# Kernel tuning notes

Measured on AMD Instinct MI355X. Metric: run time of the kernel, lower is better.

The kernel has to match this reference:

```python
import jax, jax.numpy as jnp
import numpy as np

TT_IN = (8, 8, 8, 8)
TT_OUT = (8, 8, 8, 8)
TT_RANKS = (1, 32, 32, 32, 1)
BATCH = 4096
N_IN = int(np.prod(TT_IN))     # 4096
N_OUT = int(np.prod(TT_OUT))   # 4096
KERNEL_LEN = int(sum(TT_RANKS[k] * TT_IN[k] * TT_OUT[k] * TT_RANKS[k + 1]
                     for k in range(len(TT_IN))))  # 135168


def setup_inputs() -> dict:
    key = jax.random.key(0)
    kx, kk = jax.random.split(key)
    x = jax.random.normal(kx, (BATCH, N_IN), dtype=jnp.float32)
    # flat packed TT cores (the layer stores all cores in one 1-D weight)
    kernel = 0.02 * jax.random.normal(kk, (KERNEL_LEN,), dtype=jnp.float32)
    bias = jnp.zeros((N_OUT,), dtype=jnp.float32)
    return {"x": x, "kernel": kernel, "bias": bias}


def reference(x, kernel, bias):
    # Faithful translation of TensorTrainDense.call: iterate cores k = d-1 .. 0,
    # slicing the flat kernel from index 0 (matching the original code exactly).
    batch = x.shape[0]
    res = x
    idx = 0
    for k in range(len(TT_IN) - 1, -1, -1):
        m = TT_IN[k] * TT_RANKS[k + 1]   # contraction dim
        n = TT_RANKS[k] * TT_OUT[k]      # output dim of this core
        core = kernel[idx:idx + m * n].reshape(m, n)
        res = res.reshape(-1, m) @ core              # (-1, r_k*out_k)
        res = res.reshape(-1, TT_OUT[k]).T           # (out_k, -1)
        idx += m * n
    res = res.reshape(-1, batch).T                   # (batch, prod(out))
    return res + bias
```

## Files before the change

### kernel.cpp

```cpp
#include <hip/hip_runtime.h>
#include <hip/hip_bf16.h>

typedef unsigned short u16;
typedef __attribute__((ext_vector_type(8))) short  bf16x8;
typedef __attribute__((ext_vector_type(8))) u16    u16x8;
typedef __attribute__((ext_vector_type(4))) float  fx4;

#define OFF_C0 0
#define OFF_C1 2048
#define OFF_C2 67584
#define OFF_C3 133120

static __device__ __forceinline__ u16 f2bf(float f) {
  union { __hip_bfloat16 h; u16 u; } cv;
  cv.h = __float2bfloat16(f);
  return cv.u;
}
static __device__ __forceinline__ float bf2f(u16 u) {
  union { u16 u; __hip_bfloat16 h; } cv;
  cv.u = u;
  return __bfloat162float(cv.h);
}

__global__ void build_w34T(const float* __restrict__ ker, float* __restrict__ w34T) {
  int t = blockIdx.x * 256 + threadIdx.x;
  int i34 = t & 63, c = t >> 6;
  int a2 = c >> 6, o3 = (c >> 3) & 7, o4 = c & 7;
  int i3 = i34 >> 3, i4 = i34 & 7;
  float s = 0.f;
#pragma unroll 8
  for (int a3 = 0; a3 < 32; ++a3) {
    float k1 = ker[OFF_C1 + (i3 * 32 + a3) * 256 + a2 * 8 + o3];
    float k0 = ker[OFF_C0 + i4 * 256 + a3 * 8 + o4];
    s += k1 * k0;
  }
  w34T[c * 64 + i34] = s;
}

__global__ void build_w234t2(const float* __restrict__ ker, const float* __restrict__ w34T,
                             u16* __restrict__ w234t) {
  int t = blockIdx.x * 256 + threadIdx.x;
  int i234 = t & 511, g = t >> 9;
  int a1 = g >> 3, o3 = g & 7;
  int i2 = i234 >> 6, i34 = i234 & 63;
  float acc[8][8];
#pragma unroll
  for (int a = 0; a < 8; ++a)
#pragma unroll
    for (int b = 0; b < 8; ++b) acc[a][b] = 0.f;
  for (int a2 = 0; a2 < 32; ++a2) {
    float w[8];
#pragma unroll
    for (int o4 = 0; o4 < 8; ++o4)
      w[o4] = w34T[(a2 * 64 + o3 * 8 + o4) * 64 + i34];
#pragma unroll
    for (int o2 = 0; o2 < 8; ++o2) {
      float c2 = ker[OFF_C2 + (i2 * 32 + a2) * 256 + a1 * 8 + o2];
#pragma unroll
      for (int o4 = 0; o4 < 8; ++o4) acc[o2][o4] += c2 * w[o4];
    }
  }
#pragma unroll
  for (int o2 = 0; o2 < 8; ++o2) {
    int cg = a1 * 64 + o2 * 8 + o3;
#pragma unroll
    for (int o4 = 0; o4 < 8; ++o4)
      w234t[(cg * 8 + o4) * 512 + i234] = f2bf(acc[o2][o4]);
  }
}

__global__ void build_wt2(const float* __restrict__ ker, const u16* __restrict__ w234t,
                          u16* __restrict__ wt) {
  int t = blockIdx.x * 256 + threadIdx.x;
  int i234 = t & 511, j234 = t >> 9;
  float acc[8][8];
#pragma unroll
  for (int a = 0; a < 8; ++a)
#pragma unroll
    for (int b = 0; b < 8; ++b) acc[a][b] = 0.f;
  for (int a1 = 0; a1 < 32; ++a1) {
    float w = bf2f(w234t[(a1 * 512 + j234) * 512 + i234]);
#pragma unroll
    for (int i1 = 0; i1 < 8; ++i1) {
      const float* c3 = ker + OFF_C3 + (i1 * 32 + a1) * 8;
#pragma unroll
      for (int o1 = 0; o1 < 8; ++o1) acc[i1][o1] += c3[o1] * w;
    }
  }
#pragma unroll
  for (int o1 = 0; o1 < 8; ++o1)
#pragma unroll
    for (int i1 = 0; i1 < 8; ++i1)
      wt[(size_t)(o1 * 512 + j234) * 4096 + i1 * 512 + i234] = f2bf(acc[i1][o1]);
}

__device__ __forceinline__ void gld16(const void* g, void* l) {
  __builtin_amdgcn_global_load_lds((const __attribute__((address_space(1))) void*)g,
                                   (__attribute__((address_space(3))) void*)l, 16, 0, 0);
}

__global__ __launch_bounds__(512, 2) void gemm_f32a(const float* __restrict__ X, const u16* __restrict__ Bt,
                                                    const float* __restrict__ bias, float* __restrict__ C) {
  __shared__ __align__(16) float shA[24576];
  __shared__ __align__(16) u16   shB[24576];

  const int tid = threadIdx.x;
  const int lane = tid & 63;
  const int wave = tid >> 6;
  const int wm = wave >> 2, wn = wave & 3;
  const int fr = lane & 15, fg = lane >> 4;

  const int bid = blockIdx.x;
  const int wg = (bid & 7) * 32 + (bid >> 3);
  const int bm = (wg >> 4) * 256, bn = (wg & 15) * 256;

  size_t agA[4];
#pragma unroll
  for (int L = 0; L < 4; ++L) {
    const int r = L * 64 + (tid >> 3);
    agA[L] = (size_t)(bm + r) * 4096 + (((tid & 7) ^ (r & 7)) * 4);
  }
  size_t agB[2];
#pragma unroll
  for (int L = 0; L < 2; ++L) {
    const int r = L * 128 + (tid >> 2);
    agB[L] = (size_t)(bn + r) * 4096 + (((tid & 3) ^ ((r >> 1) & 3)) * 8);
  }
  const int ldsWA = wave * 256;
  const int ldsWB = wave * 512;

  int aoff[8][2], boff[4];
#pragma unroll
  for (int m = 0; m < 8; ++m) {
    const int R = wm * 128 + m * 16 + fr;
#pragma unroll
    for (int h = 0; h < 2; ++h)
      aoff[m][h] = R * 32 + (((fg * 2 + h) ^ (R & 7)) * 4);
  }
#pragma unroll
  for (int n = 0; n < 4; ++n) {
    const int R = wn * 64 + n * 16 + fr;
    boff[n] = R * 32 + ((fg ^ ((R >> 1) & 3)) * 8);
  }

  fx4 acc[8][4];
#pragma unroll
  for (int m = 0; m < 8; ++m)
#pragma unroll
    for (int n = 0; n < 4; ++n) acc[m][n] = (fx4){0.f, 0.f, 0.f, 0.f};

#define STAGE(buf, tt) do { const int k_ = ((tt) & 127) * 32; \
    float* a_ = shA + (buf) * 8192 + ldsWA; u16* b_ = shB + (buf) * 8192 + ldsWB; \
    gld16(X + agA[0] + k_, a_); \
    gld16(X + agA[1] + k_, a_ + 2048); \
    gld16(X + agA[2] + k_, a_ + 4096); \
    gld16(X + agA[3] + k_, a_ + 6144); \
    gld16(Bt + agB[0] + k_, b_); \
    gld16(Bt + agB[1] + k_, b_ + 4096); } while (0)

  STAGE(0, 0);
  STAGE(1, 1);
  asm volatile("s_waitcnt vmcnt(6)" ::: "memory");
  __builtin_amdgcn_s_barrier();

  int p = 0;
  for (int t = 0; t < 128; ++t) {
    const int ps = p + 2 >= 3 ? p - 1 : p + 2;
    const float* Ap = shA + p * 8192;
    const u16*   Bp = shB + p * 8192;

    bf16x8 bv[4];
#pragma unroll
    for (int n = 0; n < 4; ++n) bv[n] = *(const bf16x8*)(Bp + boff[n]);

    bf16x8 av[8];
#pragma unroll
    for (int m = 0; m < 8; ++m) {
      fx4 lo = *(const fx4*)(Ap + aoff[m][0]);
      fx4 hi = *(const fx4*)(Ap + aoff[m][1]);
      u16 tmp[8];
#pragma unroll
      for (int q = 0; q < 4; ++q) tmp[q] = f2bf(lo[q]);
#pragma unroll
      for (int q = 0; q < 4; ++q) tmp[4 + q] = f2bf(hi[q]);
      av[m] = *(const bf16x8*)tmp;
    }

    STAGE(ps, t + 2);

    __builtin_amdgcn_s_setprio(1);
#pragma unroll
    for (int m = 0; m < 8; ++m)
#pragma unroll
      for (int n = 0; n < 4; ++n)
        acc[m][n] = __builtin_amdgcn_mfma_f32_16x16x32_bf16(av[m], bv[n], acc[m][n], 0, 0, 0);
    __builtin_amdgcn_s_setprio(0);

    asm volatile("s_waitcnt vmcnt(6)" ::: "memory");
    __builtin_amdgcn_s_barrier();
    p = p + 1 >= 3 ? 0 : p + 1;
  }

  const int crow0 = bm + wm * 128 + fg * 4;
  const int ccol0 = bn + wn * 64 + fr;
#pragma unroll
  for (int n = 0; n < 4; ++n) {
    const int col = ccol0 + n * 16;
    const float bvl = bias[col];
#pragma unroll
    for (int mf = 0; mf < 8; ++mf) {
      const int r0 = crow0 + mf * 16;
#pragma unroll
      for (int q = 0; q < 4; ++q)
        C[(size_t)(r0 + q) * 4096 + col] = acc[mf][n][q] + bvl;
    }
  }
#undef STAGE
}

extern "C" void kernel_launch(void* const* d_in, const int* in_sizes, int n_in,
                              void* d_out, int out_size, void* d_ws, size_t ws_size,
                              hipStream_t stream) {
  const float* x    = (const float*)d_in[0];
  const float* ker  = (const float*)d_in[1];
  const float* bias = (const float*)d_in[2];
  float* out = (float*)d_out;

  char* ws = (char*)d_ws;
  u16*  wt    = (u16*)ws;
  u16*  w234t = (u16*)(ws + 33554432);
  float* w34T = (float*)(ws + 50331648);

  build_w34T  <<<512, 256, 0, stream>>>(ker, w34T);
  build_w234t2<<<512, 256, 0, stream>>>(ker, w34T, w234t);
  build_wt2   <<<1024, 256, 0, stream>>>(ker, w234t, wt);
  gemm_f32a   <<<256, 512, 0, stream>>>(x, wt, bias, out);
}
```

Before: 192.2 us.

## Convert X tile to bf16 once on load into LDS instead of per-wave

The fp32 A tile used to be copied straight into LDS with direct-to-LDS loads, and every wave then converted its fragments to bf16 after each LDS read. Now each thread loads its fp32 slice of X into registers, converts it to bf16 once and writes it to a half-size bf16 LDS buffer, so the MFMA loop reads bf16 directly. This is meant to remove redundant conversions and halve LDS traffic and footprint for A. In exchange the A loads go through VGPRs, which adds register pressure and an extra LDS write plus lgkmcnt wait before every barrier.

```diff
diff --git a/kernel.cpp b/kernel.cpp
--- a/kernel.cpp
+++ b/kernel.cpp
@@ -99,10 +99,10 @@
                                    (__attribute__((address_space(3))) void*)l, 16, 0, 0);
 }
 
-__global__ __launch_bounds__(512, 2) void gemm_f32a(const float* __restrict__ X, const u16* __restrict__ Bt,
+__global__ __launch_bounds__(512, 2) void gemm_xf32(const float* __restrict__ X, const u16* __restrict__ Bt,
                                                     const float* __restrict__ bias, float* __restrict__ C) {
-  __shared__ __align__(16) float shA[24576];
-  __shared__ __align__(16) u16   shB[24576];
+  __shared__ __align__(16) u16 shA[24576];
+  __shared__ __align__(16) u16 shB[24576];
 
   const int tid = threadIdx.x;
   const int lane = tid & 63;
@@ -114,28 +114,23 @@
   const int wg = (bid & 7) * 32 + (bid >> 3);
   const int bm = (wg >> 4) * 256, bn = (wg & 15) * 256;
 
-  size_t agA[4];
-#pragma unroll
-  for (int L = 0; L < 4; ++L) {
-    const int r = L * 64 + (tid >> 3);
-    agA[L] = (size_t)(bm + r) * 4096 + (((tid & 7) ^ (r & 7)) * 4);
-  }
-  size_t agB[2];
-#pragma unroll
-  for (int L = 0; L < 2; ++L) {
-    const int r = L * 128 + (tid >> 2);
-    agB[L] = (size_t)(bn + r) * 4096 + (((tid & 3) ^ ((r >> 1) & 3)) * 8);
-  }
-  const int ldsWA = wave * 256;
+  const int r0 = tid >> 2, r1 = r0 + 128, sl = tid & 3;
+  const size_t aglb0 = (size_t)(bm + r0) * 4096 + (sl ^ ((r0 >> 1) & 3)) * 8;
+  const size_t aglb1 = (size_t)(bm + r1) * 4096 + (sl ^ ((r1 >> 1) & 3)) * 8;
+  const int adst0 = r0 * 32 + sl * 8;
+  const int adst1 = r1 * 32 + sl * 8;
+
+  const int srow = tid >> 2;
+  const int sco = (((tid & 3) ^ ((tid >> 3) & 3)) * 8);
+  const size_t agB0 = (size_t)(bn + srow) * 4096 + sco;
+  const size_t agB1 = agB0 + (size_t)128 * 4096;
   const int ldsWB = wave * 512;
 
-  int aoff[8][2], boff[4];
+  int aoff[8], boff[4];
 #pragma unroll
   for (int m = 0; m < 8; ++m) {
     const int R = wm * 128 + m * 16 + fr;
-#pragma unroll
-    for (int h = 0; h < 2; ++h)
-      aoff[m][h] = R * 32 + (((fg * 2 + h) ^ (R & 7)) * 4);
+    aoff[m] = R * 32 + ((fg ^ ((R >> 1) & 3)) * 8);
   }
 #pragma unroll
   for (int n = 0; n < 4; ++n) {
@@ -149,44 +144,48 @@
 #pragma unroll
     for (int n = 0; n < 4; ++n) acc[m][n] = (fx4){0.f, 0.f, 0.f, 0.f};
 
-#define STAGE(buf, tt) do { const int k_ = ((tt) & 127) * 32; \
-    float* a_ = shA + (buf) * 8192 + ldsWA; u16* b_ = shB + (buf) * 8192 + ldsWB; \
-    gld16(X + agA[0] + k_, a_); \
-    gld16(X + agA[1] + k_, a_ + 2048); \
-    gld16(X + agA[2] + k_, a_ + 4096); \
-    gld16(X + agA[3] + k_, a_ + 6144); \
-    gld16(Bt + agB[0] + k_, b_); \
-    gld16(Bt + agB[1] + k_, b_ + 4096); } while (0)
-
-  STAGE(0, 0);
-  STAGE(1, 1);
-  asm volatile("s_waitcnt vmcnt(6)" ::: "memory");
+  fx4 axl0, axh0, axl1, axh1;
+
+#define ALOAD(tt) do { const int k_ = ((tt) & 127) * 32; \
+    axl0 = *(const fx4*)(X + aglb0 + k_);  axh0 = *(const fx4*)(X + aglb0 + k_ + 4); \
+    axl1 = *(const fx4*)(X + aglb1 + k_);  axh1 = *(const fx4*)(X + aglb1 + k_ + 4); } while (0)
+#define AWRITE(buf) do { \
+    u16 t0[8], t1[8]; \
+    _Pragma("unroll") for (int q = 0; q < 4; ++q) { t0[q] = f2bf(axl0[q]); t0[4 + q] = f2bf(axh0[q]); \
+                                                    t1[q] = f2bf(axl1[q]); t1[4 + q] = f2bf(axh1[q]); } \
+    u16* ab_ = shA + (buf) * 8192; \
+    *(u16x8*)(ab_ + adst0) = *(const u16x8*)t0; \
+    *(u16x8*)(ab_ + adst1) = *(const u16x8*)t1; } while (0)
+#define STAGE_B(buf, tt) do { const int k_ = ((tt) & 127) * 32; \
+    u16* b_ = shB + (buf) * 8192 + ldsWB; \
+    gld16(Bt + agB0 + k_, b_); \
+    gld16(Bt + agB1 + k_, b_ + 4096); } while (0)
+
+  ALOAD(0);
+  STAGE_B(0, 0);
+  asm volatile("s_waitcnt vmcnt(2)" ::: "memory");
+  AWRITE(0);
+  ALOAD(1);
+  STAGE_B(1, 1);
+  asm volatile("s_waitcnt vmcnt(2)" ::: "memory");
+  AWRITE(1);
+  asm volatile("s_waitcnt lgkmcnt(0)" ::: "memory");
   __builtin_amdgcn_s_barrier();
 
   int p = 0;
   for (int t = 0; t < 128; ++t) {
-    const int ps = p + 2 >= 3 ? p - 1 : p + 2;
-    const float* Ap = shA + p * 8192;
-    const u16*   Bp = shB + p * 8192;
-
-    bf16x8 bv[4];
+    const int p2 = p + 2 >= 3 ? p - 1 : p + 2;
+    const u16* Ap = shA + p * 8192;
+    const u16* Bp = shB + p * 8192;
+
+    bf16x8 av[8], bv[4];
+#pragma unroll
+    for (int m = 0; m < 8; ++m) av[m] = *(const bf16x8*)(Ap + aoff[m]);
 #pragma unroll
     for (int n = 0; n < 4; ++n) bv[n] = *(const bf16x8*)(Bp + boff[n]);
 
-    bf16x8 av[8];
-#pragma unroll
-    for (int m = 0; m < 8; ++m) {
-      fx4 lo = *(const fx4*)(Ap + aoff[m][0]);
-      fx4 hi = *(const fx4*)(Ap + aoff[m][1]);
-      u16 tmp[8];
-#pragma unroll
-      for (int q = 0; q < 4; ++q) tmp[q] = f2bf(lo[q]);
-#pragma unroll
-      for (int q = 0; q < 4; ++q) tmp[4 + q] = f2bf(hi[q]);
-      av[m] = *(const bf16x8*)tmp;
-    }
-
-    STAGE(ps, t + 2);
+    ALOAD(t + 2);
+    STAGE_B(p2, t + 2);
 
     __builtin_amdgcn_s_setprio(1);
 #pragma unroll
@@ -196,7 +195,9 @@
         acc[m][n] = __builtin_amdgcn_mfma_f32_16x16x32_bf16(av[m], bv[n], acc[m][n], 0, 0, 0);
     __builtin_amdgcn_s_setprio(0);
 
-    asm volatile("s_waitcnt vmcnt(6)" ::: "memory");
+    asm volatile("s_waitcnt vmcnt(2)" ::: "memory");
+    AWRITE(p2);
+    asm volatile("s_waitcnt lgkmcnt(0)" ::: "memory");
     __builtin_amdgcn_s_barrier();
     p = p + 1 >= 3 ? 0 : p + 1;
   }
@@ -209,13 +210,15 @@
     const float bvl = bias[col];
 #pragma unroll
     for (int mf = 0; mf < 8; ++mf) {
-      const int r0 = crow0 + mf * 16;
+      const int r0c = crow0 + mf * 16;
 #pragma unroll
       for (int q = 0; q < 4; ++q)
-        C[(size_t)(r0 + q) * 4096 + col] = acc[mf][n][q] + bvl;
+        C[(size_t)(r0c + q) * 4096 + col] = acc[mf][n][q] + bvl;
     }
   }
-#undef STAGE
+#undef ALOAD
+#undef AWRITE
+#undef STAGE_B
 }
 
 extern "C" void kernel_launch(void* const* d_in, const int* in_sizes, int n_in,
@@ -234,5 +237,5 @@
   build_w34T  <<<512, 256, 0, stream>>>(ker, w34T);
   build_w234t2<<<512, 256, 0, stream>>>(ker, w34T, w234t);
   build_wt2   <<<1024, 256, 0, stream>>>(ker, w234t, wt);
-  gemm_f32a   <<<256, 512, 0, stream>>>(x, wt, bias, out);
-}
+  gemm_xf32   <<<256, 512, 0, stream>>>(x, wt, bias, out);
+}
```

Result: faster. 182.4 us (-5.1%).
